# Performance work log

Hardware: AMD Instinct MI355X
Metric: run time of the kernel (lower is better)

The kernel has to match this reference:

```python
import jax, jax.numpy as jnp
import numpy as np

B, N = 16, 48
NODE, EDGE, HID, MSG, LAYERS, TGT = 32, 16, 64, 64, 3, 128
NL = 128  # hidden width of cfg.net_layers / cfg.layers MLPs


def _lin(key, i, o):
    k1, k2 = jax.random.split(key)
    return (jax.random.normal(k1, (i, o), jnp.float32) * 0.05,
            jax.random.normal(k2, (o,), jnp.float32) * 0.05)


def setup_inputs() -> dict:
    key = jax.random.key(0)
    ks = jax.random.split(key, 16)
    g = (jax.random.uniform(ks[0], (B, N, N)) < 0.5).astype(jnp.float32)
    h0 = jax.random.normal(ks[1], (B, N, NODE), jnp.float32)
    e = jax.random.normal(ks[2], (B, N, N, EDGE), jnp.float32)
    msg_w0, msg_b0 = _lin(ks[3], EDGE, NL)
    msg_w1, msg_b1 = _lin(ks[4], NL, NL)
    msg_w2, msg_b2 = _lin(ks[5], NL, MSG * HID)
    gru_wih = jax.random.normal(ks[6], (3 * HID, MSG), jnp.float32) * 0.05
    gru_whh = jax.random.normal(ks[7], (3 * HID, HID), jnp.float32) * 0.05
    gru_bih = jax.random.normal(ks[8], (3 * HID,), jnp.float32) * 0.05
    gru_bhh = jax.random.normal(ks[9], (3 * HID,), jnp.float32) * 0.05
    r0_w0, r0_b0 = _lin(ks[10], 2 * HID, NL)
    r0_w1, r0_b1 = _lin(ks[11], NL, NL)
    r0_w2, r0_b2 = _lin(ks[12], NL, TGT)
    r1_w0, r1_b0 = _lin(ks[13], HID, NL)
    r1_w1, r1_b1 = _lin(ks[14], NL, NL)
    r1_w2, r1_b2 = _lin(ks[15], NL, TGT)
    return dict(g=g, h0=h0, e=e,
                msg_w0=msg_w0, msg_b0=msg_b0, msg_w1=msg_w1, msg_b1=msg_b1,
                msg_w2=msg_w2, msg_b2=msg_b2,
                gru_wih=gru_wih, gru_whh=gru_whh, gru_bih=gru_bih, gru_bhh=gru_bhh,
                r0_w0=r0_w0, r0_b0=r0_b0, r0_w1=r0_w1, r0_b1=r0_b1, r0_w2=r0_w2, r0_b2=r0_b2,
                r1_w0=r1_w0, r1_b0=r1_b0, r1_w1=r1_w1, r1_b1=r1_b1, r1_w2=r1_w2, r1_b2=r1_b2)


def _net(x, w0, b0, w1, b1, w2, b2):
    # Net: relu hidden layers, linear output (matches torch Net with 2 hidden layers)
    x = jax.nn.relu(x @ w0 + b0)
    x = jax.nn.relu(x @ w1 + b1)
    return x @ w2 + b2


def _gru_step(x, h, wih, whh, bih, bhh):
    # torch.nn.GRU single step; gate order r, z, n
    gi = x @ wih.T + bih
    gh = h @ whh.T + bhh
    r = jax.nn.sigmoid(gi[:, :HID] + gh[:, :HID])
    z = jax.nn.sigmoid(gi[:, HID:2 * HID] + gh[:, HID:2 * HID])
    n = jnp.tanh(gi[:, 2 * HID:] + r * gh[:, 2 * HID:])
    return (1.0 - z) * n + z * h


def reference(g, h0, e,
              msg_w0, msg_b0, msg_w1, msg_b1, msg_w2, msg_b2,
              gru_wih, gru_whh, gru_bih, gru_bhh,
              r0_w0, r0_b0, r0_w1, r0_b1, r0_w2, r0_b2,
              r1_w0, r1_b0, r1_w1, r1_b1, r1_w2, r1_b2):
    # pad h0 up to hidden size
    h_first = jnp.concatenate(
        [h0, jnp.zeros((B, N, HID - NODE), h0.dtype)], axis=2)
    node_mask = (jnp.sum(h0, axis=2) > 0).astype(h0.dtype)[..., None]  # [B,N,1]

    # per-edge weight matrices from edge features (same every layer in the
    # original torch code, so compute once): [B*N*N, MSG, HID]
    m_w = _net(e.reshape(-1, EDGE), msg_w0, msg_b0, msg_w1, msg_b1,
               msg_w2, msg_b2).reshape(-1, MSG, HID)

    h_t = h_first
    for _ in range(LAYERS):
        h_feat = h_t.reshape(-1, HID)  # [B*N, HID]
        # faithful to torch: expand on last dim then view(-1, HID),
        # which interleaves the hidden and neighbor axes in memory order
        h_w_rows = jnp.broadcast_to(
            h_feat[:, :, None], (B * N, HID, N)).reshape(-1, HID)
        msg = jnp.einsum('emh,eh->em', m_w, h_w_rows)  # [B*N*N, MSG]
        msg = msg.reshape(B, N, N, MSG)
        agg = jnp.sum(g[..., None] * msg, axis=1)  # masked sum over dim 1 -> [B,N,MSG]
        h_new = _gru_step(agg.reshape(-1, MSG), h_t.reshape(-1, HID),
                          gru_wih, gru_whh, gru_bih, gru_bhh).reshape(B, N, HID)
        h_t = node_mask * h_new

    # readout: Net0(cat[h_0, h_T]) * Net1(h_T), masked by h_0 activity, summed over nodes
    gate_in = jnp.concatenate([h_first, h_t], axis=-1)  # [B,N,2*HID]
    nn_res = (_net(gate_in, r0_w0, r0_b0, r0_w1, r0_b1, r0_w2, r0_b2) *
              _net(h_t, r1_w0, r1_b0, r1_w1, r1_b1, r1_w2, r1_b2))  # [B,N,TGT]
    read_mask = (jnp.sum(h_first, axis=2) > 0).astype(nn_res.dtype)[..., None]
    res = jnp.sum(read_mask * nn_res, axis=1)  # [B,TGT]
    return jax.nn.sigmoid(res)
```

## Files before the change

### kernel.cpp

```cpp
#include <hip/hip_runtime.h>
#include <cmath>

#define B_ 16
#define N_ 48
#define HID_ 64
#define NL_ 128
#define NNODE_ (B_*N_)
#define NEDGE_ (B_*N_*N_)

__device__ __forceinline__ float sigmoidf_(float x){ return 1.0f/(1.0f+expf(-x)); }

__global__ __launch_bounds__(256) void k_pm(
    const float* __restrict__ ein, const float* __restrict__ w0, const float* __restrict__ b0,
    const float* __restrict__ w1, const float* __restrict__ b1,
    const float* __restrict__ w2, const float* __restrict__ b2,
    const float* __restrict__ h0,
    const float* __restrict__ wih, const float* __restrict__ whh,
    float* __restrict__ relu2,
    float* __restrict__ A, float* __restrict__ Bm,
    float* __restrict__ Ab, float* __restrict__ Bb,
    float* __restrict__ hfirst, float* __restrict__ mask,
    float* __restrict__ wihT, float* __restrict__ whhT)
{
    __shared__ __align__(16) float x1s[64*132];
    int tid = threadIdx.x;

    if (blockIdx.x < 576){
        int et = tid & 15, ot = tid >> 4;
        int o0 = ot * 8;
        size_t e0 = (size_t)blockIdx.x * 64;

        float acc[4][8];
        {
            float4 ba = *(const float4*)&b0[o0];
            float4 bb = *(const float4*)&b0[o0 + 4];
            #pragma unroll
            for (int q = 0; q < 4; q++){
                acc[q][0]=ba.x; acc[q][1]=ba.y; acc[q][2]=ba.z; acc[q][3]=ba.w;
                acc[q][4]=bb.x; acc[q][5]=bb.y; acc[q][6]=bb.z; acc[q][7]=bb.w;
            }
        }
        #pragma unroll
        for (int i4 = 0; i4 < 4; i4++){
            float4 ev[4];
            #pragma unroll
            for (int q = 0; q < 4; q++)
                ev[q] = *(const float4*)&ein[(e0 + q*16 + et)*16 + i4*4];
            float wr[4][8];
            #pragma unroll
            for (int d = 0; d < 4; d++){
                *(float4*)&wr[d][0] = *(const float4*)&w0[(i4*4+d)*128 + o0];
                *(float4*)&wr[d][4] = *(const float4*)&w0[(i4*4+d)*128 + o0 + 4];
            }
            #pragma unroll
            for (int q = 0; q < 4; q++){
                #pragma unroll
                for (int r2 = 0; r2 < 8; r2++)
                    acc[q][r2] += ev[q].x*wr[0][r2] + ev[q].y*wr[1][r2]
                                + ev[q].z*wr[2][r2] + ev[q].w*wr[3][r2];
            }
        }
        #pragma unroll
        for (int q = 0; q < 4; q++){
            int e = q*16 + et;
            float4 s0 = make_float4(fmaxf(acc[q][0],0.f), fmaxf(acc[q][1],0.f),
                                    fmaxf(acc[q][2],0.f), fmaxf(acc[q][3],0.f));
            float4 s1 = make_float4(fmaxf(acc[q][4],0.f), fmaxf(acc[q][5],0.f),
                                    fmaxf(acc[q][6],0.f), fmaxf(acc[q][7],0.f));
            *(float4*)&x1s[e*132 + o0]     = s0;
            *(float4*)&x1s[e*132 + o0 + 4] = s1;
        }
        __syncthreads();

        float a2[4][8];
        {
            float4 ba = *(const float4*)&b1[o0];
            float4 bb = *(const float4*)&b1[o0 + 4];
            #pragma unroll
            for (int q = 0; q < 4; q++){
                a2[q][0]=ba.x; a2[q][1]=ba.y; a2[q][2]=ba.z; a2[q][3]=ba.w;
                a2[q][4]=bb.x; a2[q][5]=bb.y; a2[q][6]=bb.z; a2[q][7]=bb.w;
            }
        }
        for (int i4 = 0; i4 < 32; i4++){
            int i = i4*4;
            float wr[4][8];
            #pragma unroll
            for (int d = 0; d < 4; d++){
                *(float4*)&wr[d][0] = *(const float4*)&w1[(size_t)(i+d)*128 + o0];
                *(float4*)&wr[d][4] = *(const float4*)&w1[(size_t)(i+d)*128 + o0 + 4];
            }
            #pragma unroll
            for (int q = 0; q < 4; q++){
                float4 xv = *(const float4*)&x1s[(q*16 + et)*132 + i];
                #pragma unroll
                for (int r2 = 0; r2 < 8; r2++)
                    a2[q][r2] += xv.x*wr[0][r2] + xv.y*wr[1][r2]
                               + xv.z*wr[2][r2] + xv.w*wr[3][r2];
            }
        }
        #pragma unroll
        for (int q = 0; q < 4; q++){
            size_t e = e0 + q*16 + et;
            float4 s0 = make_float4(fmaxf(a2[q][0],0.f), fmaxf(a2[q][1],0.f),
                                    fmaxf(a2[q][2],0.f), fmaxf(a2[q][3],0.f));
            float4 s1 = make_float4(fmaxf(a2[q][4],0.f), fmaxf(a2[q][5],0.f),
                                    fmaxf(a2[q][6],0.f), fmaxf(a2[q][7],0.f));
            *(float4*)&relu2[e*128 + o0]     = s0;
            *(float4*)&relu2[e*128 + o0 + 4] = s1;
        }
    } else {
        int idx = (blockIdx.x - 576)*256 + tid;
        if (idx < 24576) {
            int r = idx >> 13, c = (idx >> 6) & 127, m = idx & 63;
            int t = 48 - 16*r;
            const float* src = w2 + c*4096 + m*64;
            float a = 0.f, b = 0.f;
            #pragma unroll
            for (int k4 = 0; k4 < 16; k4++){
                float4 v = *(const float4*)&src[k4*4];
                float s = v.x + v.y + v.z + v.w;
                if (k4*4 < t) a += s; else b += s;
            }
            A[idx] = a; Bm[idx] = b;
        } else if (idx < 24768) {
            int i2 = idx - 24576;
            int r = i2 >> 6, m = i2 & 63;
            int t = 48 - 16*r;
            const float* src = b2 + m*64;
            float a = 0.f, b = 0.f;
            #pragma unroll
            for (int k4 = 0; k4 < 16; k4++){
                float4 v = *(const float4*)&src[k4*4];
                float s = v.x + v.y + v.z + v.w;
                if (k4*4 < t) a += s; else b += s;
            }
            Ab[i2] = a; Bb[i2] = b;
        } else if (idx < 73920) {
            int i3 = idx - 24768;
            int node = i3 >> 6, m = i3 & 63;
            hfirst[i3] = (m < 32) ? h0[node*32 + m] : 0.f;
            if (m == 0) {
                float s = 0.f;
                #pragma unroll
                for (int k = 0; k < 32; k++) s += h0[node*32 + k];
                mask[node] = (s > 0.f) ? 1.f : 0.f;
            }
        } else if (idx < 98496) {
            int i4 = idx - 73920;
            if (i4 < 12288) {
                int k = i4 / 192, col = i4 - k*192;
                wihT[i4] = wih[col*64 + k];
            } else {
                int i5 = i4 - 12288;
                int k = i5 / 192, col = i5 - k*192;
                whhT[i5] = whh[col*64 + k];
            }
        }
    }
}

__global__ __launch_bounds__(256) void k_layer(
    const float* __restrict__ hin, float* __restrict__ hout,
    const float* __restrict__ relu2,
    const float* __restrict__ A, const float* __restrict__ Bm,
    const float* __restrict__ Ab, const float* __restrict__ Bb,
    const float* __restrict__ g, const float* __restrict__ mask,
    const float* __restrict__ wihT, const float* __restrict__ whhT,
    const float* __restrict__ bih, const float* __restrict__ bhh)
{
    int bj = blockIdx.x;
    int b = bj / 48, j = bj - b*48;
    int r = j % 3;
    int p0 = j + j/3;
    int tid = threadIdx.x;
    int base = b*48;
    __shared__ __align__(16) float r2s[48*128];
    __shared__ float hs[64], wAs[64], wBs[64], Abs[64], Bbs[64];
    __shared__ float pU[2][128], pV[2][128];
    __shared__ float pC[4][64];
    __shared__ float aggs[64], gi[192], gh[192];
    __shared__ float sAB[2];

    {
        const float* src = relu2 + ((size_t)base*48 + j)*128;
        #pragma unroll
        for (int q2 = 0; q2 < 6; q2++){
            int flat = q2*256 + tid;
            int row = flat >> 5, col = (flat & 31)*4;
            float4 v = *(const float4*)&src[(size_t)row*6144 + col];
            *(float4*)&r2s[row*128 + col] = v;
        }
    }
    if (tid < 64){
        hs[tid] = hin[(size_t)bj*64 + tid];
    } else if (tid < 128){
        int i = tid - 64;
        float wa = 0.f, wb = 0.f;
        if (i < 48){
            float gv = g[(size_t)(base+i)*48 + j];
            wa = gv * hin[(size_t)(base+i)*64 + p0];
            wb = gv * hin[(size_t)(base+i)*64 + p0 + 1];
        }
        wAs[i] = wa; wBs[i] = wb;
        float sa = wa, sb = wb;
        #pragma unroll
        for (int d = 32; d >= 1; d >>= 1){
            sa += __shfl_xor(sa, d, 64);
            sb += __shfl_xor(sb, d, 64);
        }
        if (i == 0){ sAB[0] = sa; sAB[1] = sb; }
    } else if (tid < 192){
        Bbs[tid-128] = Bb[r*64 + (tid-128)];
    } else {
        Abs[tid-192] = Ab[r*64 + (tid-192)];
    }
    __syncthreads();

    {
        int c = tid & 127, half = tid >> 7;
        float aU = 0.f, aV = 0.f;
        #pragma unroll
        for (int ii = 0; ii < 24; ii++){
            int i = half*24 + ii;
            float v = r2s[i*128 + c];
            aU += wAs[i]*v; aV += wBs[i]*v;
        }
        pU[half][c] = aU; pV[half][c] = aV;
    }
    __syncthreads();

    {
        int m = tid & 63, cg = tid >> 6;
        const float* Arp = A  + r*8192 + m;
        const float* Brp = Bm + r*8192 + m;
        float a = 0.f;
        #pragma unroll
        for (int cc = 0; cc < 32; cc++){
            int c = cg*32 + cc;
            float u = pU[0][c] + pU[1][c];
            float v = pV[0][c] + pV[1][c];
            a += u*Arp[(size_t)c*64] + v*Brp[(size_t)c*64];
        }
        pC[cg][m] = a;
    }
    __syncthreads();

    if (tid < 64){
        aggs[tid] = pC[0][tid] + pC[1][tid] + pC[2][tid] + pC[3][tid]
                  + sAB[0]*Abs[tid] + sAB[1]*Bbs[tid];
    }
    __syncthreads();

    if (tid < 192){
        float gacc = bih[tid], hacc = bhh[tid];
        #pragma unroll 16
        for (int k = 0; k < 64; k++){
            gacc += aggs[k] * wihT[k*192 + tid];
            hacc += hs[k]   * whhT[k*192 + tid];
        }
        gi[tid] = gacc; gh[tid] = hacc;
    }
    __syncthreads();

    if (tid < 64){
        float rr = sigmoidf_(gi[tid] + gh[tid]);
        float zz = sigmoidf_(gi[64+tid] + gh[64+tid]);
        float nn = tanhf(gi[128+tid] + rr*gh[128+tid]);
        float hnew = (1.f - zz)*nn + zz*hs[tid];
        hout[(size_t)bj*64 + tid] = mask[bj] * hnew;
    }
}

__device__ __forceinline__ void stage_w(const float* __restrict__ W,
                                        float* __restrict__ Ws, int rows, int tid)
{
    for (int f = tid; f < rows*32; f += 256){
        int i = f >> 5, c4 = (f & 31) << 2;
        *(float4*)&Ws[i*129 + c4] = *(const float4*)&W[(size_t)i*128 + c4];
    }
}

__device__ __forceinline__ void lds_layer(const float* __restrict__ Ws,
    const float* __restrict__ xsrc,
    const float* __restrict__ bias, float* __restrict__ dst,
    int dim, int o, int ng, bool do_relu)
{
    float a0 = bias[o];
    float a1 = a0;
    #pragma unroll 8
    for (int k = 0; k < dim; k += 4){
        float4 x0 = *(const float4*)&xsrc[ng*132 + k];
        float4 x1 = *(const float4*)&xsrc[(ng+2)*132 + k];
        float w0 = Ws[(k+0)*129 + o];
        float w1 = Ws[(k+1)*129 + o];
        float w2 = Ws[(k+2)*129 + o];
        float w3 = Ws[(k+3)*129 + o];
        a0 += x0.x*w0 + x0.y*w1 + x0.z*w2 + x0.w*w3;
        a1 += x1.x*w0 + x1.y*w1 + x1.z*w2 + x1.w*w3;
    }
    if (do_relu){ a0 = fmaxf(a0, 0.f); a1 = fmaxf(a1, 0.f); }
    dst[ng*132 + o] = a0;
    dst[(ng+2)*132 + o] = a1;
}

__global__ __launch_bounds__(256) void k_read(
    const float* __restrict__ hfirst, const float* __restrict__ hT,
    const float* __restrict__ mask,
    const float* __restrict__ w00, const float* __restrict__ b00,
    const float* __restrict__ w01, const float* __restrict__ b01,
    const float* __restrict__ w02, const float* __restrict__ b02,
    const float* __restrict__ w10, const float* __restrict__ b10,
    const float* __restrict__ w11, const float* __restrict__ b11,
    const float* __restrict__ w12, const float* __restrict__ b12,
    float* __restrict__ partial)
{
    __shared__ __align__(16) float Ws[128*129];
    __shared__ __align__(16) float xs[4*132], ys[4*132], zs[4*132], os0[4*132];
    __shared__ float mS[4];
    int tid = threadIdx.x;
    int b = blockIdx.x / 12, gg = blockIdx.x - b*12;
    int node0 = b*48 + gg*4;
    int o = tid & 127, ng = tid >> 7;

    if (tid < 4) mS[tid] = mask[node0 + tid];
    for (int i = tid; i < 4*128; i += 256){
        int r = i >> 7, c = i & 127;
        xs[r*132 + c] = (c < 64) ? hfirst[(size_t)(node0+r)*64 + c]
                                 : hT[(size_t)(node0+r)*64 + (c - 64)];
    }
    stage_w(w00, Ws, 128, tid);                       __syncthreads();
    lds_layer(Ws, xs,      b00, ys,  128, o, ng, true);  __syncthreads();
    stage_w(w01, Ws, 128, tid);                       __syncthreads();
    lds_layer(Ws, ys,      b01, zs,  128, o, ng, true);  __syncthreads();
    stage_w(w02, Ws, 128, tid);                       __syncthreads();
    lds_layer(Ws, zs,      b02, os0, 128, o, ng, false); __syncthreads();
    stage_w(w10, Ws, 64, tid);                        __syncthreads();
    lds_layer(Ws, xs + 64, b10, ys,  64,  o, ng, true);  __syncthreads();
    stage_w(w11, Ws, 128, tid);                       __syncthreads();
    lds_layer(Ws, ys,      b11, zs,  128, o, ng, true);  __syncthreads();
    stage_w(w12, Ws, 128, tid);                       __syncthreads();
    {
        float a0 = b12[o];
        float a1 = a0;
        #pragma unroll 8
        for (int k = 0; k < 128; k += 4){
            float4 x0 = *(const float4*)&zs[ng*132 + k];
            float4 x1 = *(const float4*)&zs[(ng+2)*132 + k];
            float w0 = Ws[(k+0)*129 + o];
            float w1 = Ws[(k+1)*129 + o];
            float w2 = Ws[(k+2)*129 + o];
            float w3 = Ws[(k+3)*129 + o];
            a0 += x0.x*w0 + x0.y*w1 + x0.z*w2 + x0.w*w3;
            a1 += x1.x*w0 + x1.y*w1 + x1.z*w2 + x1.w*w3;
        }
        float s = mS[ng]   * os0[ng*132 + o]     * a0
                + mS[ng+2] * os0[(ng+2)*132 + o] * a1;
        __syncthreads();
        ys[ng*132 + o] = s;
    }
    __syncthreads();
    if (tid < 128)
        partial[(size_t)blockIdx.x*128 + tid] = ys[tid] + ys[132 + tid];
}

__global__ void k_final(const float* __restrict__ partial, float* __restrict__ out)
{
    int idx = blockIdx.x*256 + threadIdx.x;
    if (idx < B_*128){
        int b = idx >> 7, t = idx & 127;
        float s = 0.f;
        #pragma unroll
        for (int c = 0; c < 12; c++) s += partial[(size_t)(b*12 + c)*128 + t];
        out[idx] = 1.0f / (1.0f + expf(-s));
    }
}

extern "C" void kernel_launch(void* const* d_in, const int* in_sizes, int n_in,
                              void* d_out, int out_size, void* d_ws, size_t ws_size,
                              hipStream_t stream)
{
    (void)in_sizes; (void)n_in; (void)out_size; (void)ws_size;
    const float* g    = (const float*)d_in[0];
    const float* h0   = (const float*)d_in[1];
    const float* e    = (const float*)d_in[2];
    const float* mw0  = (const float*)d_in[3];
    const float* mb0  = (const float*)d_in[4];
    const float* mw1  = (const float*)d_in[5];
    const float* mb1  = (const float*)d_in[6];
    const float* mw2  = (const float*)d_in[7];
    const float* mb2  = (const float*)d_in[8];
    const float* wih  = (const float*)d_in[9];
    const float* whh  = (const float*)d_in[10];
    const float* bih  = (const float*)d_in[11];
    const float* bhh  = (const float*)d_in[12];
    const float* r0w0 = (const float*)d_in[13];
    const float* r0b0 = (const float*)d_in[14];
    const float* r0w1 = (const float*)d_in[15];
    const float* r0b1 = (const float*)d_in[16];
    const float* r0w2 = (const float*)d_in[17];
    const float* r0b2 = (const float*)d_in[18];
    const float* r1w0 = (const float*)d_in[19];
    const float* r1b0 = (const float*)d_in[20];
    const float* r1w1 = (const float*)d_in[21];
    const float* r1b1 = (const float*)d_in[22];
    const float* r1w2 = (const float*)d_in[23];
    const float* r1b2 = (const float*)d_in[24];
    float* out = (float*)d_out;

    float* ws     = (float*)d_ws;
    float* A      = ws;
    float* Bm     = A      + 24576;
    float* Ab     = Bm     + 24576;
    float* Bb     = Ab     + 192;
    float* hfirst = Bb     + 192;
    float* hA     = hfirst + 49152;
    float* hB     = hA     + 49152;
    float* mask   = hB     + 49152;
    float* wihT   = mask   + 768;
    float* whhT   = wihT   + 12288;
    float* part   = whhT   + 12288;
    float* relu2  = part   + 24576;

    k_pm<<<961, 256, 0, stream>>>(e, mw0, mb0, mw1, mb1, mw2, mb2, h0, wih, whh,
                                  relu2, A, Bm, Ab, Bb, hfirst, mask, wihT, whhT);
    k_layer<<<768, 256, 0, stream>>>(hfirst, hA, relu2, A, Bm, Ab, Bb, g, mask,
                                     wihT, whhT, bih, bhh);
    k_layer<<<768, 256, 0, stream>>>(hA, hB, relu2, A, Bm, Ab, Bb, g, mask,
                                     wihT, whhT, bih, bhh);
    k_layer<<<768, 256, 0, stream>>>(hB, hA, relu2, A, Bm, Ab, Bb, g, mask,
                                     wihT, whhT, bih, bhh);
    k_read<<<192, 256, 0, stream>>>(hfirst, hA, mask,
                                    r0w0, r0b0, r0w1, r0b1, r0w2, r0b2,
                                    r1w0, r1b0, r1w1, r1b1, r1w2, r1b2, part);
    k_final<<<8, 256, 0, stream>>>(part, out);
}
```

Before: 206.1 us.

## Fuse three GRU layer launches into one persistent kernel with grid barrier

```diff
diff --git a/kernel.cpp b/kernel.cpp
--- a/kernel.cpp
+++ b/kernel.cpp
@@ -10,7 +10,7 @@
 
 __device__ __forceinline__ float sigmoidf_(float x){ return 1.0f/(1.0f+expf(-x)); }
 
-__global__ __launch_bounds__(256) void k_pm(
+__global__ __launch_bounds__(256, 3) void k_pm(
     const float* __restrict__ ein, const float* __restrict__ w0, const float* __restrict__ b0,
     const float* __restrict__ w1, const float* __restrict__ b1,
     const float* __restrict__ w2, const float* __restrict__ b2,
@@ -82,21 +82,32 @@
                 a2[q][4]=bb.x; a2[q][5]=bb.y; a2[q][6]=bb.z; a2[q][7]=bb.w;
             }
         }
+        float4 wb2[2][8];
+        #pragma unroll
+        for (int d = 0; d < 4; d++){
+            wb2[0][d*2]   = *(const float4*)&w1[(size_t)d*128 + o0];
+            wb2[0][d*2+1] = *(const float4*)&w1[(size_t)d*128 + o0 + 4];
+        }
+        #pragma unroll 2
         for (int i4 = 0; i4 < 32; i4++){
+            int cur = i4 & 1;
+            if (i4 < 31){
+                int inx = (i4+1)*4;
+                #pragma unroll
+                for (int d = 0; d < 4; d++){
+                    wb2[cur^1][d*2]   = *(const float4*)&w1[(size_t)(inx+d)*128 + o0];
+                    wb2[cur^1][d*2+1] = *(const float4*)&w1[(size_t)(inx+d)*128 + o0 + 4];
+                }
+            }
             int i = i4*4;
-            float wr[4][8];
-            #pragma unroll
-            for (int d = 0; d < 4; d++){
-                *(float4*)&wr[d][0] = *(const float4*)&w1[(size_t)(i+d)*128 + o0];
-                *(float4*)&wr[d][4] = *(const float4*)&w1[(size_t)(i+d)*128 + o0 + 4];
-            }
+            const float* wcur = (const float*)&wb2[cur][0];
             #pragma unroll
             for (int q = 0; q < 4; q++){
                 float4 xv = *(const float4*)&x1s[(q*16 + et)*132 + i];
                 #pragma unroll
                 for (int r2 = 0; r2 < 8; r2++)
-                    a2[q][r2] += xv.x*wr[0][r2] + xv.y*wr[1][r2]
-                               + xv.z*wr[2][r2] + xv.w*wr[3][r2];
+                    a2[q][r2] += xv.x*wcur[0*8+r2] + xv.y*wcur[1*8+r2]
+                               + xv.z*wcur[2*8+r2] + xv.w*wcur[3*8+r2];
             }
         }
         #pragma unroll
@@ -160,14 +171,15 @@
     }
 }
 
-__global__ __launch_bounds__(256) void k_layer(
-    const float* __restrict__ hin, float* __restrict__ hout,
+__global__ __launch_bounds__(256, 3) void k_layers(
+    const float* __restrict__ hfirst, float* __restrict__ hA, float* __restrict__ hB,
     const float* __restrict__ relu2,
     const float* __restrict__ A, const float* __restrict__ Bm,
     const float* __restrict__ Ab, const float* __restrict__ Bb,
     const float* __restrict__ g, const float* __restrict__ mask,
     const float* __restrict__ wihT, const float* __restrict__ whhT,
-    const float* __restrict__ bih, const float* __restrict__ bhh)
+    const float* __restrict__ bih, const float* __restrict__ bhh,
+    unsigned* __restrict__ bar)
 {
     int bj = blockIdx.x;
     int b = bj / 48, j = bj - b*48;
@@ -176,6 +188,7 @@
     int tid = threadIdx.x;
     int base = b*48;
     __shared__ __align__(16) float r2s[48*128];
+    __shared__ float gs[48];
     __shared__ float hs[64], wAs[64], wBs[64], Abs[64], Bbs[64];
     __shared__ float pU[2][128], pV[2][128];
     __shared__ float pC[4][64];
@@ -192,92 +205,117 @@
             *(float4*)&r2s[row*128 + col] = v;
         }
     }
-    if (tid < 64){
-        hs[tid] = hin[(size_t)bj*64 + tid];
-    } else if (tid < 128){
-        int i = tid - 64;
-        float wa = 0.f, wb = 0.f;
-        if (i < 48){
-            float gv = g[(size_t)(base+i)*48 + j];
-            wa = gv * hin[(size_t)(base+i)*64 + p0];
-            wb = gv * hin[(size_t)(base+i)*64 + p0 + 1];
-        }
-        wAs[i] = wa; wBs[i] = wb;
-        float sa = wa, sb = wb;
-        #pragma unroll
-        for (int d = 32; d >= 1; d >>= 1){
-            sa += __shfl_xor(sa, d, 64);
-            sb += __shfl_xor(sb, d, 64);
-        }
-        if (i == 0){ sAB[0] = sa; sAB[1] = sb; }
-    } else if (tid < 192){
-        Bbs[tid-128] = Bb[r*64 + (tid-128)];
-    } else {
-        Abs[tid-192] = Ab[r*64 + (tid-192)];
-    }
+    if (tid < 48) gs[tid] = g[(size_t)(base+tid)*48 + j];
+    else if (tid >= 128 && tid < 192) Bbs[tid-128] = Bb[r*64 + (tid-128)];
+    else if (tid >= 192) Abs[tid-192] = Ab[r*64 + (tid-192)];
     __syncthreads();
 
-    {
-        int c = tid & 127, half = tid >> 7;
-        float aU = 0.f, aV = 0.f;
-        #pragma unroll
-        for (int ii = 0; ii < 24; ii++){
-            int i = half*24 + ii;
-            float v = r2s[i*128 + c];
-            aU += wAs[i]*v; aV += wBs[i]*v;
-        }
-        pU[half][c] = aU; pV[half][c] = aV;
-    }
-    __syncthreads();
-
-    {
-        int m = tid & 63, cg = tid >> 6;
-        const float* Arp = A  + r*8192 + m;
-        const float* Brp = Bm + r*8192 + m;
-        float a = 0.f;
-        #pragma unroll
-        for (int cc = 0; cc < 32; cc++){
-            int c = cg*32 + cc;
-            float u = pU[0][c] + pU[1][c];
-            float v = pV[0][c] + pV[1][c];
-            a += u*Arp[(size_t)c*64] + v*Brp[(size_t)c*64];
-        }
-        pC[cg][m] = a;
-    }
-    __syncthreads();
-
-    if (tid < 64){
-        aggs[tid] = pC[0][tid] + pC[1][tid] + pC[2][tid] + pC[3][tid]
-                  + sAB[0]*Abs[tid] + sAB[1]*Bbs[tid];
-    }
-    __syncthreads();
-
-    if (tid < 192){
-        float gacc = bih[tid], hacc = bhh[tid];
-        #pragma unroll 16
-        for (int k = 0; k < 64; k++){
-            gacc += aggs[k] * wihT[k*192 + tid];
-            hacc += hs[k]   * whhT[k*192 + tid];
-        }
-        gi[tid] = gacc; gh[tid] = hacc;
-    }
-    __syncthreads();
-
-    if (tid < 64){
-        float rr = sigmoidf_(gi[tid] + gh[tid]);
-        float zz = sigmoidf_(gi[64+tid] + gh[64+tid]);
-        float nn = tanhf(gi[128+tid] + rr*gh[128+tid]);
-        float hnew = (1.f - zz)*nn + zz*hs[tid];
-        hout[(size_t)bj*64 + tid] = mask[bj] * hnew;
-    }
-}
-
-__device__ __forceinline__ void stage_w(const float* __restrict__ W,
-                                        float* __restrict__ Ws, int rows, int tid)
-{
-    for (int f = tid; f < rows*32; f += 256){
-        int i = f >> 5, c4 = (f & 31) << 2;
-        *(float4*)&Ws[i*129 + c4] = *(const float4*)&W[(size_t)i*128 + c4];
+    const float* hin = hfirst;
+    for (int L = 0; L < 3; L++){
+        float* hout = (L == 0) ? hA : (L == 1) ? hB : hA;
+
+        if (tid < 64){
+            hs[tid] = hin[(size_t)bj*64 + tid];
+        } else if (tid < 128){
+            int i = tid - 64;
+            float wa = 0.f, wb = 0.f;
+            if (i < 48){
+                float gv = gs[i];
+                wa = gv * hin[(size_t)(base+i)*64 + p0];
+                wb = gv * hin[(size_t)(base+i)*64 + p0 + 1];
+            }
+            wAs[i] = wa; wBs[i] = wb;
+            float sa = wa, sb = wb;
+            #pragma unroll
+            for (int d = 32; d >= 1; d >>= 1){
+                sa += __shfl_xor(sa, d, 64);
+                sb += __shfl_xor(sb, d, 64);
+            }
+            if (i == 0){ sAB[0] = sa; sAB[1] = sb; }
+        }
+        __syncthreads();
+
+        {
+            int c = tid & 127, half = tid >> 7;
+            float aU = 0.f, aV = 0.f;
+            #pragma unroll
+            for (int ii = 0; ii < 24; ii++){
+                int i = half*24 + ii;
+                float v = r2s[i*128 + c];
+                aU += wAs[i]*v; aV += wBs[i]*v;
+            }
+            pU[half][c] = aU; pV[half][c] = aV;
+        }
+        __syncthreads();
+
+        {
+            int m = tid & 63, cg = tid >> 6;
+            const float* Arp = A  + r*8192 + m;
+            const float* Brp = Bm + r*8192 + m;
+            float a = 0.f;
+            #pragma unroll
+            for (int cc = 0; cc < 32; cc++){
+                int c = cg*32 + cc;
+                float u = pU[0][c] + pU[1][c];
+                float v = pV[0][c] + pV[1][c];
+                a += u*Arp[(size_t)c*64] + v*Brp[(size_t)c*64];
+            }
+            pC[cg][m] = a;
+        }
+        __syncthreads();
+
+        if (tid < 64){
+            aggs[tid] = pC[0][tid] + pC[1][tid] + pC[2][tid] + pC[3][tid]
+                      + sAB[0]*Abs[tid] + sAB[1]*Bbs[tid];
+        }
+        __syncthreads();
+
+        if (tid < 192){
+            float gacc = bih[tid], hacc = bhh[tid];
+            #pragma unroll 16
+            for (int k = 0; k < 64; k++){
+                gacc += aggs[k] * wihT[k*192 + tid];
+                hacc += hs[k]   * whhT[k*192 + tid];
+            }
+            gi[tid] = gacc; gh[tid] = hacc;
+        }
+        __syncthreads();
+
+        if (tid < 64){
+            float rr = sigmoidf_(gi[tid] + gh[tid]);
+            float zz = sigmoidf_(gi[64+tid] + gh[64+tid]);
+            float nn = tanhf(gi[128+tid] + rr*gh[128+tid]);
+            float hnew = (1.f - zz)*nn + zz*hs[tid];
+            hout[(size_t)bj*64 + tid] = mask[bj] * hnew;
+        }
+
+        if (L < 2){
+            __syncthreads();
+            if (tid == 0){
+                __threadfence();
+                atomicAdd(bar, 1u);
+                unsigned target = (unsigned)(L + 1) * (unsigned)gridDim.x;
+                while (__hip_atomic_load(bar, __ATOMIC_RELAXED,
+                                         __HIP_MEMORY_SCOPE_AGENT) < target) { }
+                __threadfence();
+            }
+            __syncthreads();
+        }
+        hin = hout;
+    }
+}
+
+__device__ __forceinline__ void stage_w_fast(const float* __restrict__ W,
+                                             float* __restrict__ Ws, int n4, int tid)
+{
+    for (int base = tid; base < n4; base += 2048){
+        float4 tmp[8];
+        #pragma unroll
+        for (int s = 0; s < 8; s++)
+            tmp[s] = *(const float4*)&W[(size_t)(base + s*256)*4];
+        #pragma unroll
+        for (int s = 0; s < 8; s++)
+            *(float4*)&Ws[(size_t)(base + s*256)*4] = tmp[s];
     }
 }
 
@@ -292,10 +330,10 @@
     for (int k = 0; k < dim; k += 4){
         float4 x0 = *(const float4*)&xsrc[ng*132 + k];
         float4 x1 = *(const float4*)&xsrc[(ng+2)*132 + k];
-        float w0 = Ws[(k+0)*129 + o];
-        float w1 = Ws[(k+1)*129 + o];
-        float w2 = Ws[(k+2)*129 + o];
-        float w3 = Ws[(k+3)*129 + o];
+        float w0 = Ws[(k+0)*128 + o];
+        float w1 = Ws[(k+1)*128 + o];
+        float w2 = Ws[(k+2)*128 + o];
+        float w3 = Ws[(k+3)*128 + o];
         a0 += x0.x*w0 + x0.y*w1 + x0.z*w2 + x0.w*w3;
         a1 += x1.x*w0 + x1.y*w1 + x1.z*w2 + x1.w*w3;
     }
@@ -304,7 +342,7 @@
     dst[(ng+2)*132 + o] = a1;
 }
 
-__global__ __launch_bounds__(256) void k_read(
+__global__ __launch_bounds__(256, 2) void k_read(
     const float* __restrict__ hfirst, const float* __restrict__ hT,
     const float* __restrict__ mask,
     const float* __restrict__ w00, const float* __restrict__ b00,
@@ -315,7 +353,7 @@
     const float* __restrict__ w12, const float* __restrict__ b12,
     float* __restrict__ partial)
 {
-    __shared__ __align__(16) float Ws[128*129];
+    __shared__ __align__(16) float Ws[128*128];
     __shared__ __align__(16) float xs[4*132], ys[4*132], zs[4*132], os0[4*132];
     __shared__ float mS[4];
     int tid = threadIdx.x;
@@ -329,17 +367,17 @@
         xs[r*132 + c] = (c < 64) ? hfirst[(size_t)(node0+r)*64 + c]
                                  : hT[(size_t)(node0+r)*64 + (c - 64)];
     }
-    stage_w(w00, Ws, 128, tid);                       __syncthreads();
+    stage_w_fast(w00, Ws, 4096, tid);                   __syncthreads();
     lds_layer(Ws, xs,      b00, ys,  128, o, ng, true);  __syncthreads();
-    stage_w(w01, Ws, 128, tid);                       __syncthreads();
+    stage_w_fast(w01, Ws, 4096, tid);                   __syncthreads();
     lds_layer(Ws, ys,      b01, zs,  128, o, ng, true);  __syncthreads();
-    stage_w(w02, Ws, 128, tid);                       __syncthreads();
+    stage_w_fast(w02, Ws, 4096, tid);                   __syncthreads();
     lds_layer(Ws, zs,      b02, os0, 128, o, ng, false); __syncthreads();
-    stage_w(w10, Ws, 64, tid);                        __syncthreads();
+    stage_w_fast(w10, Ws, 2048, tid);                   __syncthreads();
     lds_layer(Ws, xs + 64, b10, ys,  64,  o, ng, true);  __syncthreads();
-    stage_w(w11, Ws, 128, tid);                       __syncthreads();
+    stage_w_fast(w11, Ws, 4096, tid);                   __syncthreads();
     lds_layer(Ws, ys,      b11, zs,  128, o, ng, true);  __syncthreads();
-    stage_w(w12, Ws, 128, tid);                       __syncthreads();
+    stage_w_fast(w12, Ws, 4096, tid);                   __syncthreads();
     {
         float a0 = b12[o];
         float a1 = a0;
@@ -347,10 +385,10 @@
         for (int k = 0; k < 128; k += 4){
             float4 x0 = *(const float4*)&zs[ng*132 + k];
             float4 x1 = *(const float4*)&zs[(ng+2)*132 + k];
-            float w0 = Ws[(k+0)*129 + o];
-            float w1 = Ws[(k+1)*129 + o];
-            float w2 = Ws[(k+2)*129 + o];
-            float w3 = Ws[(k+3)*129 + o];
+            float w0 = Ws[(k+0)*128 + o];
+            float w1 = Ws[(k+1)*128 + o];
+            float w2 = Ws[(k+2)*128 + o];
+            float w3 = Ws[(k+3)*128 + o];
             a0 += x0.x*w0 + x0.y*w1 + x0.z*w2 + x0.w*w3;
             a1 += x1.x*w0 + x1.y*w1 + x1.z*w2 + x1.w*w3;
         }
@@ -420,16 +458,14 @@
     float* wihT   = mask   + 768;
     float* whhT   = wihT   + 12288;
     float* part   = whhT   + 12288;
-    float* relu2  = part   + 24576;
-
+    unsigned* bar = (unsigned*)(part + 24576);
+    float* relu2  = part   + 24576 + 16;
+
+    hipMemsetAsync(bar, 0, 16, stream);
     k_pm<<<961, 256, 0, stream>>>(e, mw0, mb0, mw1, mb1, mw2, mb2, h0, wih, whh,
                                   relu2, A, Bm, Ab, Bb, hfirst, mask, wihT, whhT);
-    k_layer<<<768, 256, 0, stream>>>(hfirst, hA, relu2, A, Bm, Ab, Bb, g, mask,
-                                     wihT, whhT, bih, bhh);
-    k_layer<<<768, 256, 0, stream>>>(hA, hB, relu2, A, Bm, Ab, Bb, g, mask,
-                                     wihT, whhT, bih, bhh);
-    k_layer<<<768, 256, 0, stream>>>(hB, hA, relu2, A, Bm, Ab, Bb, g, mask,
-                                     wihT, whhT, bih, bhh);
+    k_layers<<<768, 256, 0, stream>>>(hfirst, hA, hB, relu2, A, Bm, Ab, Bb,
+                                      g, mask, wihT, whhT, bih, bhh, bar);
     k_read<<<192, 256, 0, stream>>>(hfirst, hA, mask,
                                     r0w0, r0b0, r0w1, r0b1, r0w2, r0b2,
                                     r1w0, r1b0, r1w1, r1b1, r1w2, r1b2, part);
```

Measured after the change: 333.8 us. 62.0% more time.
